# Kernel tuning notes

Hardware: AMD Instinct MI355X
Metric: run time of the kernel (lower is better)

The kernel has to match this reference:

```python
import jax, jax.numpy as jnp
import numpy as np

HEADS = 16
HEAD_DIM = 64

def setup_inputs() -> dict:
    key = jax.random.key(0)
    ks = jax.random.split(key, 5)
    S, B, H = 1024, 4, 1024
    scale = 1.0 / np.sqrt(H)
    return {
        "hidden_states": jax.random.normal(ks[0], (S, B, H), jnp.float32),
        "attention_mask": jnp.zeros((B * HEADS, 1, S), jnp.float32),
        "Wq": jax.random.normal(ks[1], (H, H), jnp.float32) * scale,
        "bq": jnp.zeros((H,), jnp.float32),
        "Wk": jax.random.normal(ks[2], (H, H), jnp.float32) * scale,
        "bk": jnp.zeros((H,), jnp.float32),
        "Wv": jax.random.normal(ks[3], (H, H), jnp.float32) * scale,
        "bv": jnp.zeros((H,), jnp.float32),
    }

def reference(hidden_states, attention_mask, Wq, bq, Wk, bk, Wv, bv):
    S, B, H = hidden_states.shape
    d = HEAD_DIM
    inv_sqrt_d = 1.0 / np.sqrt(d)
    # QKV projections (torch Linear: x @ W.T + b)
    q = hidden_states @ Wq.T + bq  # (S, B, H)
    k = hidden_states @ Wk.T + bk
    v = hidden_states @ Wv.T + bv
    # (S, B*heads, d) -> (B*heads, S, d)
    q = q.reshape(S, B * HEADS, d).transpose(1, 0, 2)
    k = k.reshape(S, B * HEADS, d).transpose(1, 0, 2)
    v = v.reshape(S, B * HEADS, d).transpose(1, 0, 2)
    # SDDMM: scaled scores + additive mask -> (B*heads, S, S)
    scores = jnp.einsum('nsd,ntd->nst', q, k) * inv_sqrt_d + attention_mask
    probs = jax.nn.softmax(scores, axis=-1)
    # AV bmm -> (B*heads, S, d); note: dropout in source is seeded but never applied
    ctx = jnp.einsum('nst,ntd->nsd', probs, v)
    # back to (S, B, hidden)
    ctx = ctx.transpose(1, 0, 2).reshape(S, B, H)
    return ctx
```

## Files before the change

### kernel.cpp

```cpp
#include <hip/hip_runtime.h>
#include <hip/hip_bf16.h>
#include <math.h>

#define S_LEN 1024
#define BATCH 4
#define HID 1024
#define NHEADS 16
#define DHEAD 64
#define NTOT 64
#define M_ROWS 4096

typedef unsigned short u16;
typedef unsigned int u32;
typedef __bf16 bf16x8 __attribute__((ext_vector_type(8)));
typedef float f32x4 __attribute__((ext_vector_type(4)));

__device__ __forceinline__ u16 f2bf(float x) {
    __hip_bfloat16 h = __float2bfloat16(x);
    return *(u16*)&h;
}

__device__ __forceinline__ void gll16(const u16* g, u16* l) {
    __builtin_amdgcn_global_load_lds(
        (const __attribute__((address_space(1))) u32*)g,
        (__attribute__((address_space(3))) u32*)l, 16, 0, 0);
}

__global__ __launch_bounds__(256) void cvt_all(
    const float* __restrict__ X, const float* __restrict__ wq,
    const float* __restrict__ wk, const float* __restrict__ wv,
    u16* __restrict__ Xb, u16* __restrict__ Wb)
{
    const int bid = blockIdx.x;
    const float* src;
    u16* dst;
    size_t off;
    if (bid < 4096) {
        src = X; dst = Xb; off = (size_t)bid * 1024;
    } else {
        const int wb = bid - 4096;
        const int which = wb >> 10;
        src = (which == 0) ? wq : (which == 1) ? wk : wv;
        dst = Wb + (size_t)which * HID * HID;
        off = (size_t)(wb & 1023) * 1024;
    }
    const size_t idx = off + threadIdx.x * 4;
    float4 x = *(const float4*)(src + idx);
    *(ushort4*)(dst + idx) = make_ushort4(f2bf(x.x), f2bf(x.y), f2bf(x.z), f2bf(x.w));
}

__global__ __launch_bounds__(256, 3) void qkv_mfma(
    const u16* __restrict__ Xb, const u16* __restrict__ Wb,
    const float* __restrict__ bq, const float* __restrict__ bk,
    const float* __restrict__ bv,
    u16* __restrict__ Qb, u16* __restrict__ Kb, u16* __restrict__ VT)
{
    const int m0 = blockIdx.x * 128;
    const int n0 = blockIdx.y * 128;
    const int which = blockIdx.z;

    __shared__ __align__(16) u16 As[128 * 32];
    __shared__ __align__(16) u16 Bs[128 * 32];

    const int tid = threadIdx.x;
    const int lane = tid & 63;
    const int w = tid >> 6;
    const int wm = w & 1, wn = w >> 1;
    const int quad = lane >> 4;
    const int l15 = lane & 15;

    const u16* W = Wb + (size_t)which * HID * HID;

    f32x4 acc[4][4];
    #pragma unroll
    for (int i = 0; i < 4; ++i)
        #pragma unroll
        for (int j = 0; j < 4; ++j)
            #pragma unroll
            for (int r = 0; r < 4; ++r) acc[i][j][r] = 0.0f;

    const int lrow = lane >> 2, lchk = (lane & 3) * 8;

    for (int k0 = 0; k0 < HID; k0 += 32) {
        #pragma unroll
        for (int c = 0; c < 2; ++c) {
            const int seg = w * 2 + c;
            const int row = seg * 16 + lrow;
            gll16(Xb + (size_t)(m0 + row) * HID + k0 + lchk, As + seg * 512);
            gll16(W  + (size_t)(n0 + row) * HID + k0 + lchk, Bs + seg * 512);
        }
        __syncthreads();

        bf16x8 af[4], bf[4];
        #pragma unroll
        for (int i = 0; i < 4; ++i)
            af[i] = *(const bf16x8*)(As + (wm * 64 + i * 16 + l15) * 32 + quad * 8);
        #pragma unroll
        for (int j = 0; j < 4; ++j)
            bf[j] = *(const bf16x8*)(Bs + (wn * 64 + j * 16 + l15) * 32 + quad * 8);
        #pragma unroll
        for (int i = 0; i < 4; ++i)
            #pragma unroll
            for (int j = 0; j < 4; ++j)
                acc[i][j] = __builtin_amdgcn_mfma_f32_16x16x32_bf16(
                    af[i], bf[j], acc[i][j], 0, 0, 0);
        __syncthreads();
    }

    const float* bias = (which == 0) ? bq : (which == 1) ? bk : bv;
    #pragma unroll
    for (int j = 0; j < 4; ++j) {
        const int o = n0 + wn * 64 + j * 16 + l15;
        const float bias_v = bias[o];
        const int head = o >> 6, d = o & 63;
        #pragma unroll
        for (int i = 0; i < 4; ++i) {
            const int mbase = m0 + wm * 64 + i * 16 + quad * 4;
            const int s = mbase >> 2;
            #pragma unroll
            for (int r = 0; r < 4; ++r) {
                const int n = r * NHEADS + head;
                const u16 hv = f2bf(acc[i][j][r] + bias_v);
                if (which == 0)
                    Qb[((size_t)n * S_LEN + s) * DHEAD + d] = hv;
                else if (which == 1)
                    Kb[((size_t)n * S_LEN + s) * DHEAD + d] = hv;
                else
                    VT[(size_t)n * (DHEAD * S_LEN) + (size_t)d * S_LEN + s] = hv;
            }
        }
    }
}

__global__ __launch_bounds__(256, 2) void attn_mfma(
    const u16* __restrict__ Qb, const u16* __restrict__ Kb,
    const u16* __restrict__ VT, const float* __restrict__ mask,
    float* __restrict__ out)
{
    const int n = blockIdx.y;
    const int s0 = blockIdx.x * 128;
    const int b = n >> 4, head = n & 15;

    __shared__ __align__(16) char smem[51200];
    u16* Kbuf = (u16*)smem;
    u16* Vbuf = (u16*)(smem + 16384);
    u16* Ps   = (u16*)(smem + 32768);
    float* Of = (float*)smem;

    const int tid = threadIdx.x;
    const int lane = tid & 63;
    const int w = tid >> 6;
    const int quad = lane >> 4;
    const int l15 = lane & 15;
    const size_t nbase = (size_t)n * S_LEN * DHEAD;

    const int xs0 = ((quad ^ (l15 & 7)) * 8);
    const int xs1 = (((4 + quad) ^ (l15 & 7)) * 8);

    const int srow = lane >> 3;
    const int scg  = (lane & 7) ^ (srow & 7);

    bf16x8 qf[2][2];
    #pragma unroll
    for (int mi = 0; mi < 2; ++mi)
        #pragma unroll
        for (int st = 0; st < 2; ++st)
            qf[mi][st] = *(const bf16x8*)(Qb + nbase +
                (size_t)(s0 + w * 32 + mi * 16 + l15) * 64 + st * 32 + quad * 8);

    f32x4 O[2][4];
    float l_lane[2];
    #pragma unroll
    for (int mi = 0; mi < 2; ++mi) {
        l_lane[mi] = 0.0f;
        #pragma unroll
        for (int jt = 0; jt < 4; ++jt)
            #pragma unroll
            for (int r = 0; r < 4; ++r) O[mi][jt][r] = 0.0f;
    }

    {
        #pragma unroll
        for (int c = 0; c < 2; ++c) {
            const int seg = w * 2 + c;
            const int row = seg * 8 + srow;
            gll16(Kb + nbase + (size_t)row * 64 + scg * 8, Kbuf + seg * 512);
            gll16(VT + nbase + (size_t)row * S_LEN + scg * 8, Vbuf + seg * 512);
        }
    }
    __syncthreads();

    for (int it = 0; it < 16; ++it) {
        const int t0 = it * 64;
        const u16* kb = Kbuf + (it & 1) * 4096;
        const u16* vb = Vbuf + (it & 1) * 4096;

        if (it < 15) {
            u16* kd = Kbuf + ((it + 1) & 1) * 4096;
            u16* vd = Vbuf + ((it + 1) & 1) * 4096;
            #pragma unroll
            for (int c = 0; c < 2; ++c) {
                const int seg = w * 2 + c;
                const int row = seg * 8 + srow;
                gll16(Kb + nbase + (size_t)(t0 + 64 + row) * 64 + scg * 8, kd + seg * 512);
                gll16(VT + nbase + (size_t)row * S_LEN + t0 + 64 + scg * 8, vd + seg * 512);
            }
        }

        f32x4 sc[2][4];
        #pragma unroll
        for (int mi = 0; mi < 2; ++mi)
            #pragma unroll
            for (int j = 0; j < 4; ++j)
                #pragma unroll
                for (int r = 0; r < 4; ++r) sc[mi][j][r] = 0.0f;

        #pragma unroll
        for (int st = 0; st < 2; ++st) {
            const int xo = st ? xs1 : xs0;
            bf16x8 kf[4];
            #pragma unroll
            for (int j = 0; j < 4; ++j)
                kf[j] = *(const bf16x8*)(kb + (j * 16 + l15) * 64 + xo);
            #pragma unroll
            for (int mi = 0; mi < 2; ++mi)
                #pragma unroll
                for (int j = 0; j < 4; ++j)
                    sc[mi][j] = __builtin_amdgcn_mfma_f32_16x16x32_bf16(
                        kf[j], qf[mi][st], sc[mi][j], 0, 0, 0);
        }

        float4 mv4[4];
        #pragma unroll
        for (int j = 0; j < 4; ++j)
            mv4[j] = *(const float4*)(mask + (size_t)n * S_LEN + t0 + j * 16 + quad * 4);

        #pragma unroll
        for (int mi = 0; mi < 2; ++mi) {
            const int q = w * 32 + mi * 16 + l15;
            #pragma unroll
            for (int j = 0; j < 4; ++j) {
                const float p0 = __expf(fmaf(sc[mi][j][0], 0.125f, mv4[j].x - 16.0f));
                const float p1 = __expf(fmaf(sc[mi][j][1], 0.125f, mv4[j].y - 16.0f));
                const float p2 = __expf(fmaf(sc[mi][j][2], 0.125f, mv4[j].z - 16.0f));
                const float p3 = __expf(fmaf(sc[mi][j][3], 0.125f, mv4[j].w - 16.0f));
                l_lane[mi] += (p0 + p1) + (p2 + p3);
                *(ushort4*)(Ps + q * 72 + j * 16 + quad * 4) =
                    make_ushort4(f2bf(p0), f2bf(p1), f2bf(p2), f2bf(p3));
            }
        }

        #pragma unroll
        for (int st = 0; st < 2; ++st) {
            const int xo = st ? xs1 : xs0;
            bf16x8 vf[4];
            #pragma unroll
            for (int jt = 0; jt < 4; ++jt)
                vf[jt] = *(const bf16x8*)(vb + (jt * 16 + l15) * 64 + xo);
            #pragma unroll
            for (int mi = 0; mi < 2; ++mi) {
                bf16x8 pf = *(const bf16x8*)(Ps + (w * 32 + mi * 16 + l15) * 72 +
                                             st * 32 + quad * 8);
                #pragma unroll
                for (int jt = 0; jt < 4; ++jt)
                    O[mi][jt] = __builtin_amdgcn_mfma_f32_16x16x32_bf16(
                        vf[jt], pf, O[mi][jt], 0, 0, 0);
            }
        }

        __syncthreads();
    }

    float inv_l[2];
    #pragma unroll
    for (int mi = 0; mi < 2; ++mi) {
        float l = l_lane[mi];
        l += __shfl_xor(l, 16);
        l += __shfl_xor(l, 32);
        inv_l[mi] = 1.0f / l;
    }
    __syncthreads();

    #pragma unroll
    for (int mi = 0; mi < 2; ++mi) {
        const int q = w * 32 + mi * 16 + l15;
        #pragma unroll
        for (int jt = 0; jt < 4; ++jt)
            #pragma unroll
            for (int r = 0; r < 4; ++r)
                Of[q * 72 + jt * 16 + quad * 4 + r] = O[mi][jt][r] * inv_l[mi];
    }
    __syncthreads();

    const int tx = tid & 15, ty = tid >> 4;
    #pragma unroll
    for (int p = 0; p < 8; ++p) {
        const int q = p * 16 + ty;
        float4 v = *(const float4*)(Of + q * 72 + tx * 4);
        *(float4*)(out + (size_t)(s0 + q) * (BATCH * HID) + (size_t)b * HID +
                   head * DHEAD + tx * 4) = v;
    }
}

extern "C" void kernel_launch(void* const* d_in, const int* in_sizes, int n_in,
                              void* d_out, int out_size, void* d_ws, size_t ws_size,
                              hipStream_t stream)
{
    const float* X    = (const float*)d_in[0];
    const float* mask = (const float*)d_in[1];
    const float* Wq   = (const float*)d_in[2];
    const float* bq   = (const float*)d_in[3];
    const float* Wk   = (const float*)d_in[4];
    const float* bk   = (const float*)d_in[5];
    const float* Wv   = (const float*)d_in[6];
    const float* bv   = (const float*)d_in[7];
    float* out = (float*)d_out;

    const size_t MX = (size_t)M_ROWS * HID;
    const size_t MW = (size_t)HID * HID;
    u16* wsp = (u16*)d_ws;
    u16* Xb = wsp;
    u16* Wb = Xb + MX;
    u16* Qb = Wb + 3 * MW;
    u16* Kb = Qb + MX;
    u16* VT = Kb + MX;

    cvt_all<<<dim3(4096 + 3072), 256, 0, stream>>>(X, Wq, Wk, Wv, Xb, Wb);
    qkv_mfma<<<dim3(M_ROWS / 128, HID / 128, 3), 256, 0, stream>>>(
        Xb, Wb, bq, bk, bv, Qb, Kb, VT);
    attn_mfma<<<dim3(S_LEN / 128, NTOT), 256, 0, stream>>>(Qb, Kb, VT, mask, out);
}
```

Measured before the change: 159.4 us.

## Deepen QKV GEMM K-tile with swizzled LDS, exp2 softmax, setprio, block remap

The QKV GEMM now loads 64-wide K tiles into an XOR-swizzled LDS layout, which halves the number of barriers per K and avoids bank conflicts. The attention kernel switches from expf to a native exp2 by folding log2e into the scale and mask offset. It also raises wave priority around the MFMA sections and flattens the grid with a swizzled block-to-(head, query tile) mapping to change CU scheduling. The doubled LDS tiles in the GEMM may affect occupancy.

```diff
diff --git a/kernel.cpp b/kernel.cpp
--- a/kernel.cpp
+++ b/kernel.cpp
@@ -18,6 +18,14 @@
 __device__ __forceinline__ u16 f2bf(float x) {
     __hip_bfloat16 h = __float2bfloat16(x);
     return *(u16*)&h;
+}
+
+__device__ __forceinline__ float fexp2(float x) {
+#if __has_builtin(__builtin_amdgcn_exp2f)
+    return __builtin_amdgcn_exp2f(x);
+#else
+    return __expf(x * 0.6931471805599453f);
+#endif
 }
 
 __device__ __forceinline__ void gll16(const u16* g, u16* l) {
@@ -59,8 +67,8 @@
     const int n0 = blockIdx.y * 128;
     const int which = blockIdx.z;
 
-    __shared__ __align__(16) u16 As[128 * 32];
-    __shared__ __align__(16) u16 Bs[128 * 32];
+    __shared__ __align__(16) u16 As[128 * 64];
+    __shared__ __align__(16) u16 Bs[128 * 64];
 
     const int tid = threadIdx.x;
     const int lane = tid & 63;
@@ -68,6 +76,7 @@
     const int wm = w & 1, wn = w >> 1;
     const int quad = lane >> 4;
     const int l15 = lane & 15;
+    const int r7 = l15 & 7;
 
     const u16* W = Wb + (size_t)which * HID * HID;
 
@@ -79,31 +88,36 @@
             #pragma unroll
             for (int r = 0; r < 4; ++r) acc[i][j][r] = 0.0f;
 
-    const int lrow = lane >> 2, lchk = (lane & 3) * 8;
-
-    for (int k0 = 0; k0 < HID; k0 += 32) {
-        #pragma unroll
-        for (int c = 0; c < 2; ++c) {
-            const int seg = w * 2 + c;
-            const int row = seg * 16 + lrow;
-            gll16(Xb + (size_t)(m0 + row) * HID + k0 + lchk, As + seg * 512);
-            gll16(W  + (size_t)(n0 + row) * HID + k0 + lchk, Bs + seg * 512);
+    const int srow = lane >> 3;
+    const int scg  = ((lane & 7) ^ srow) * 8;
+
+    for (int k0 = 0; k0 < HID; k0 += 64) {
+        #pragma unroll
+        for (int c = 0; c < 4; ++c) {
+            const int seg = w * 4 + c;
+            const int row = seg * 8 + srow;
+            gll16(Xb + (size_t)(m0 + row) * HID + k0 + scg, As + seg * 512);
+            gll16(W  + (size_t)(n0 + row) * HID + k0 + scg, Bs + seg * 512);
         }
         __syncthreads();
 
-        bf16x8 af[4], bf[4];
-        #pragma unroll
-        for (int i = 0; i < 4; ++i)
-            af[i] = *(const bf16x8*)(As + (wm * 64 + i * 16 + l15) * 32 + quad * 8);
-        #pragma unroll
-        for (int j = 0; j < 4; ++j)
-            bf[j] = *(const bf16x8*)(Bs + (wn * 64 + j * 16 + l15) * 32 + quad * 8);
-        #pragma unroll
-        for (int i = 0; i < 4; ++i)
+        #pragma unroll
+        for (int kk = 0; kk < 2; ++kk) {
+            const int xo = ((kk * 4 + quad) ^ r7) * 8;
+            bf16x8 af[4], bf[4];
+            #pragma unroll
+            for (int i = 0; i < 4; ++i)
+                af[i] = *(const bf16x8*)(As + (wm * 64 + i * 16 + l15) * 64 + xo);
             #pragma unroll
             for (int j = 0; j < 4; ++j)
-                acc[i][j] = __builtin_amdgcn_mfma_f32_16x16x32_bf16(
-                    af[i], bf[j], acc[i][j], 0, 0, 0);
+                bf[j] = *(const bf16x8*)(Bs + (wn * 64 + j * 16 + l15) * 64 + xo);
+            #pragma unroll
+            for (int i = 0; i < 4; ++i)
+                #pragma unroll
+                for (int j = 0; j < 4; ++j)
+                    acc[i][j] = __builtin_amdgcn_mfma_f32_16x16x32_bf16(
+                        af[i], bf[j], acc[i][j], 0, 0, 0);
+        }
         __syncthreads();
     }
 
@@ -137,8 +151,10 @@
     const u16* __restrict__ VT, const float* __restrict__ mask,
     float* __restrict__ out)
 {
-    const int n = blockIdx.y;
-    const int s0 = blockIdx.x * 128;
+    const int bid = blockIdx.x;
+    const int swz = (bid & 7) * 64 + (bid >> 3);
+    const int n = swz >> 3;
+    const int s0 = (swz & 7) * 128;
     const int b = n >> 4, head = n & 15;
 
     __shared__ __align__(16) char smem[51200];
@@ -190,6 +206,10 @@
     }
     __syncthreads();
 
+    const float LOG2E = 1.44269504f;
+    const float SCL2  = 0.18033688f;
+    const float MOFF  = -23.0831099f;
+
     for (int it = 0; it < 16; ++it) {
         const int t0 = it * 64;
         const u16* kb = Kbuf + (it & 1) * 4096;
@@ -215,6 +235,7 @@
                 #pragma unroll
                 for (int r = 0; r < 4; ++r) sc[mi][j][r] = 0.0f;
 
+        __builtin_amdgcn_s_setprio(1);
         #pragma unroll
         for (int st = 0; st < 2; ++st) {
             const int xo = st ? xs1 : xs0;
@@ -229,27 +250,34 @@
                     sc[mi][j] = __builtin_amdgcn_mfma_f32_16x16x32_bf16(
                         kf[j], qf[mi][st], sc[mi][j], 0, 0, 0);
         }
-
-        float4 mv4[4];
-        #pragma unroll
-        for (int j = 0; j < 4; ++j)
-            mv4[j] = *(const float4*)(mask + (size_t)n * S_LEN + t0 + j * 16 + quad * 4);
+        __builtin_amdgcn_s_setprio(0);
+
+        float4 mb4[4];
+        #pragma unroll
+        for (int j = 0; j < 4; ++j) {
+            float4 mv = *(const float4*)(mask + (size_t)n * S_LEN + t0 + j * 16 + quad * 4);
+            mb4[j].x = fmaf(mv.x, LOG2E, MOFF);
+            mb4[j].y = fmaf(mv.y, LOG2E, MOFF);
+            mb4[j].z = fmaf(mv.z, LOG2E, MOFF);
+            mb4[j].w = fmaf(mv.w, LOG2E, MOFF);
+        }
 
         #pragma unroll
         for (int mi = 0; mi < 2; ++mi) {
             const int q = w * 32 + mi * 16 + l15;
             #pragma unroll
             for (int j = 0; j < 4; ++j) {
-                const float p0 = __expf(fmaf(sc[mi][j][0], 0.125f, mv4[j].x - 16.0f));
-                const float p1 = __expf(fmaf(sc[mi][j][1], 0.125f, mv4[j].y - 16.0f));
-                const float p2 = __expf(fmaf(sc[mi][j][2], 0.125f, mv4[j].z - 16.0f));
-                const float p3 = __expf(fmaf(sc[mi][j][3], 0.125f, mv4[j].w - 16.0f));
+                const float p0 = fexp2(fmaf(sc[mi][j][0], SCL2, mb4[j].x));
+                const float p1 = fexp2(fmaf(sc[mi][j][1], SCL2, mb4[j].y));
+                const float p2 = fexp2(fmaf(sc[mi][j][2], SCL2, mb4[j].z));
+                const float p3 = fexp2(fmaf(sc[mi][j][3], SCL2, mb4[j].w));
                 l_lane[mi] += (p0 + p1) + (p2 + p3);
                 *(ushort4*)(Ps + q * 72 + j * 16 + quad * 4) =
                     make_ushort4(f2bf(p0), f2bf(p1), f2bf(p2), f2bf(p3));
             }
         }
 
+        __builtin_amdgcn_s_setprio(1);
         #pragma unroll
         for (int st = 0; st < 2; ++st) {
             const int xo = st ? xs1 : xs0;
@@ -267,6 +295,7 @@
                         vf[jt], pf, O[mi][jt], 0, 0, 0);
             }
         }
+        __builtin_amdgcn_s_setprio(0);
 
         __syncthreads();
     }
@@ -328,5 +357,5 @@
     cvt_all<<<dim3(4096 + 3072), 256, 0, stream>>>(X, Wq, Wk, Wv, Xb, Wb);
     qkv_mfma<<<dim3(M_ROWS / 128, HID / 128, 3), 256, 0, stream>>>(
         Xb, Wb, bq, bk, bv, Qb, Kb, VT);
-    attn_mfma<<<dim3(S_LEN / 128, NTOT), 256, 0, stream>>>(Qb, Kb, VT, mask, out);
-}
+    attn_mfma<<<dim3(S_LEN / 128 * NTOT), 256, 0, stream>>>(Qb, Kb, VT, mask, out);
+}
```

Result: faster. 149.2 us (-6.4%).
